# Kernel optimization log

Measured on AMD Instinct MI355X. Metric: run time of the kernel, lower is better.

Reference implementation:

```python
import jax, jax.numpy as jnp
import numpy as np

N = 100_000   # nodes
E = 3_200_000 # edges
B = 64        # graphs in batch
OUT = 64      # config


def setup_inputs() -> dict:
    key = jax.random.key(0)
    ks = jax.random.split(key, 12)
    x = jax.random.normal(ks[0], (N, 3), dtype=jnp.float32)
    edge_index = jax.random.randint(ks[1], (2, E), 0, N, dtype=jnp.int32)
    batch = jnp.sort(jax.random.randint(ks[2], (N,), 0, B, dtype=jnp.int32))
    # GCNConv weights (PyG: out = norm_adj @ (x @ W) + b)
    W1 = jax.random.normal(ks[3], (3, 32), dtype=jnp.float32) * 0.5
    b1 = jnp.zeros((32,), dtype=jnp.float32)
    W2 = jax.random.normal(ks[4], (32, 32), dtype=jnp.float32) * 0.18
    b2 = jnp.zeros((32,), dtype=jnp.float32)
    LW1 = jax.random.normal(ks[5], (64, 64), dtype=jnp.float32) * 0.125
    Lb1 = jnp.zeros((64,), dtype=jnp.float32)
    LW2 = jax.random.normal(ks[6], (64, OUT), dtype=jnp.float32) * 0.125
    Lb2 = jnp.zeros((OUT,), dtype=jnp.float32)
    return {"x": x, "edge_index": edge_index, "batch": batch,
            "W1": W1, "b1": b1, "W2": W2, "b2": b2,
            "LW1": LW1, "Lb1": Lb1, "LW2": LW2, "Lb2": Lb2}


def _gcn_norm(edge_index, n):
    # add self-loops, compute symmetric normalization D^-1/2 (A+I) D^-1/2
    loops = jnp.arange(n, dtype=edge_index.dtype)
    src = jnp.concatenate([edge_index[0], loops])
    dst = jnp.concatenate([edge_index[1], loops])
    deg = jax.ops.segment_sum(jnp.ones_like(dst, dtype=jnp.float32), dst,
                              num_segments=n)
    dinv = jnp.where(deg > 0, 1.0 / jnp.sqrt(deg), 0.0)
    norm = dinv[src] * dinv[dst]  # [E+N]
    return src, dst, norm


def _gcn_conv(x, W, b, src, dst, norm, n):
    h = x @ W                         # [N, F_out] tiny GEMM
    m = h[src] * norm[:, None]        # edge gather  [E+N, F_out]
    out = jax.ops.segment_sum(m, dst, num_segments=n)  # scatter-add
    return out + b


def _pool(x, batch, nb):
    # cat(global_max_pool, global_mean_pool)
    mx = jax.ops.segment_max(x, batch, num_segments=nb)
    sm = jax.ops.segment_sum(x, batch, num_segments=nb)
    cnt = jax.ops.segment_sum(jnp.ones((x.shape[0],), x.dtype), batch,
                              num_segments=nb)
    mean = sm / jnp.maximum(cnt, 1.0)[:, None]
    return jnp.concatenate([mx, mean], axis=1)


def reference(x, edge_index, batch, W1, b1, W2, b2, LW1, Lb1, LW2, Lb2):
    n = x.shape[0]
    src, dst, norm = _gcn_norm(edge_index, n)
    h = jax.nn.relu(_gcn_conv(x, W1, b1, src, dst, norm, n))
    x1 = _pool(h, batch, B)           # [B, 64]
    h2 = jax.nn.relu(_gcn_conv(h, W2, b2, src, dst, norm, n))
    x2 = _pool(h2, batch, B)          # [B, 64]
    z = jax.nn.relu((x1 + x2) @ LW1 + Lb1)
    # dropout p=0.5 skipped (eval mode / training=False)
    out = z @ LW2 + Lb2               # [B, OUT]; .squeeze(1) is a no-op for OUT>1
    return out
```

## Files before the change

### kernel.cpp

```cpp
#include <hip/hip_runtime.h>
#include <hip/hip_fp16.h>


#define F 32
#define POOLD 64
#define BKT 512
#define BKTL2 9
#define EPB 8192
#define MAXBUCK 256

typedef __attribute__((ext_vector_type(8))) _Float16 half8;

__global__ void k_histB(const int* __restrict__ ei, int* __restrict__ bcnt,
                        int e, int nbuck, int nblk) {
    __shared__ int h[MAXBUCK];
    for (int b = threadIdx.x; b < nbuck; b += 256) h[b] = 0;
    __syncthreads();
    int base = blockIdx.x * EPB;
#pragma unroll
    for (int k = 0; k < EPB / 1024; ++k) {
        int i = base + (k * 256 + threadIdx.x) * 4;
        if (i + 4 <= e) {
            int4 d4 = *reinterpret_cast<const int4*>(ei + e + i);
            atomicAdd(&h[d4.x >> BKTL2], 1);
            atomicAdd(&h[d4.y >> BKTL2], 1);
            atomicAdd(&h[d4.z >> BKTL2], 1);
            atomicAdd(&h[d4.w >> BKTL2], 1);
        } else {
            for (int j = i; j < e && j < i + 4; ++j)
                atomicAdd(&h[ei[e + j] >> BKTL2], 1);
        }
    }
    __syncthreads();
    for (int b = threadIdx.x; b < nbuck; b += 256)
        bcnt[b * nblk + blockIdx.x] = h[b];
}

__global__ void k_rowscan(int* __restrict__ bcnt, int* __restrict__ tot, int nblk) {
    __shared__ int lds[256];
    int* row = bcnt + (size_t)blockIdx.x * nblk;
    int t = threadIdx.x;
    int running = 0;
    for (int chunk = 0; chunk < nblk; chunk += 256) {
        int idx = chunk + t;
        int v = (idx < nblk) ? row[idx] : 0;
        lds[t] = v;
        __syncthreads();
        int val = v;
        for (int off = 1; off < 256; off <<= 1) {
            int other = (t >= off) ? lds[t - off] : 0;
            __syncthreads();
            val += other;
            lds[t] = val;
            __syncthreads();
        }
        if (idx < nblk) row[idx] = running + val - v;
        running += lds[255];
        __syncthreads();
    }
    if (t == 0) tot[blockIdx.x] = running;
}

__global__ void k_bscan(const int* __restrict__ tot, int* __restrict__ bstart,
                        int nbuck, int e) {
    __shared__ int lds[256];
    int t = threadIdx.x;
    int v = (t < nbuck) ? tot[t] : 0;
    lds[t] = v;
    __syncthreads();
    int val = v;
    for (int off = 1; off < 256; off <<= 1) {
        int other = (t >= off) ? lds[t - off] : 0;
        __syncthreads();
        val += other;
        lds[t] = val;
        __syncthreads();
    }
    if (t < nbuck) bstart[t] = val - v;
    if (t == 0) bstart[nbuck] = e;
}

__global__ void k_bin(const int* __restrict__ ei, const int* __restrict__ bstart,
                      const int* __restrict__ bcnt, int* __restrict__ packed,
                      int e, int nbuck, int nblk) {
    __shared__ int cur[MAXBUCK];
    for (int b = threadIdx.x; b < nbuck; b += 256)
        cur[b] = bstart[b] + bcnt[b * nblk + blockIdx.x];
    __syncthreads();
    int base = blockIdx.x * EPB;
#pragma unroll
    for (int k = 0; k < EPB / 1024; ++k) {
        int i = base + (k * 256 + threadIdx.x) * 4;
        if (i + 4 <= e) {
            int4 s4 = *reinterpret_cast<const int4*>(ei + i);
            int4 d4 = *reinterpret_cast<const int4*>(ei + e + i);
            int p0 = atomicAdd(&cur[d4.x >> BKTL2], 1);
            int p1 = atomicAdd(&cur[d4.y >> BKTL2], 1);
            int p2 = atomicAdd(&cur[d4.z >> BKTL2], 1);
            int p3 = atomicAdd(&cur[d4.w >> BKTL2], 1);
            packed[p0] = (s4.x << BKTL2) | (d4.x & (BKT - 1));
            packed[p1] = (s4.y << BKTL2) | (d4.y & (BKT - 1));
            packed[p2] = (s4.z << BKTL2) | (d4.z & (BKT - 1));
            packed[p3] = (s4.w << BKTL2) | (d4.w & (BKT - 1));
        } else {
            for (int j = i; j < e && j < i + 4; ++j) {
                int s = ei[j], d = ei[e + j];
                int p = atomicAdd(&cur[d >> BKTL2], 1);
                packed[p] = (s << BKTL2) | (d & (BKT - 1));
            }
        }
    }
}

__global__ void k_place2(const int* __restrict__ packed, const int* __restrict__ bstart,
                         int* __restrict__ col, int* __restrict__ rp,
                         float* __restrict__ dinv, int n) {
    __shared__ int deg[BKT];
    __shared__ int sc[BKT];
    __shared__ int cur[BKT];
    int t = threadIdx.x;
    deg[t] = 0;
    __syncthreads();
    int start = bstart[blockIdx.x];
    int end = bstart[blockIdx.x + 1];
    for (int i = start + t; i < end; i += BKT)
        atomicAdd(&deg[packed[i] & (BKT - 1)], 1);
    __syncthreads();
    int d0 = deg[t];
    sc[t] = d0;
    __syncthreads();
    int val = d0;
    for (int off = 1; off < BKT; off <<= 1) {
        int other = (t >= off) ? sc[t - off] : 0;
        __syncthreads();
        val += other;
        sc[t] = val;
        __syncthreads();
    }
    int node = blockIdx.x * BKT + t;
    int ex = start + val - d0;
    if (node < n) {
        rp[node] = ex;
        dinv[node] = rsqrtf((float)d0 + 1.0f);
    }
    cur[t] = ex;
    __syncthreads();
    for (int i = start + t; i < end; i += BKT) {
        int u = packed[i];
        int p = atomicAdd(&cur[u & (BKT - 1)], 1);
        col[p] = u >> BKTL2;
    }
}

__global__ void k_xw1(const float* __restrict__ x, const float* __restrict__ W1,
                      _Float16* __restrict__ p0, _Float16* __restrict__ p1, int n) {
    int i = blockIdx.x * blockDim.x + threadIdx.x;
    if (i >= n * F) return;
    int node = i >> 5, f = i & (F - 1);
    float x0 = x[node * 3 + 0], x1 = x[node * 3 + 1], x2 = x[node * 3 + 2];
    float v = x0 * W1[f] + x1 * W1[F + f] + x2 * W1[2 * F + f];
    _Float16* plane = (f < 16) ? p0 : p1;
    plane[node * 16 + (f & 15)] = (_Float16)v;
}

__global__ void k_gemm2(const _Float16* __restrict__ h0, const _Float16* __restrict__ h1,
                        const float* __restrict__ W2,
                        _Float16* __restrict__ g0, _Float16* __restrict__ g1, int n) {
    int i = blockIdx.x * blockDim.x + threadIdx.x;
    if (i >= n * F) return;
    int node = i >> 5, f = i & (F - 1);
    const _Float16* r0 = h0 + (size_t)node * 16;
    const _Float16* r1 = h1 + (size_t)node * 16;
    float acc = 0.0f;
#pragma unroll
    for (int k = 0; k < 16; ++k) acc += (float)r0[k] * W2[k * F + f];
#pragma unroll
    for (int k = 0; k < 16; ++k) acc += (float)r1[k] * W2[(k + 16) * F + f];
    _Float16* plane = (f < 16) ? g0 : g1;
    plane[node * 16 + (f & 15)] = (_Float16)acc;
}

__global__ void k_gather(const _Float16* __restrict__ plane, const int* __restrict__ rp,
                         const int* __restrict__ col, const float* __restrict__ dinv,
                         const float* __restrict__ bias, const int* __restrict__ batch,
                         _Float16* __restrict__ outPlane,
                         float* __restrict__ psum, float* __restrict__ pmax,
                         float* __restrict__ cnt, int n, int ne, int fh,
                         int store, int do_cnt) {
    int t = blockIdx.x * blockDim.x + threadIdx.x;
    int node = t >> 1, q = t & 1;
    if (node >= n) return;
    int start = rp[node];
    int end = (node + 1 < n) ? rp[node + 1] : ne;
    float dv = dinv[node];

    half8 hv = *reinterpret_cast<const half8*>(plane + (size_t)node * 16 + q * 8);
    float dvv = dv * dv;
    float acc[8];
#pragma unroll
    for (int j = 0; j < 8; ++j) acc[j] = (float)hv[j] * dvv;

    int e = start;
    for (; e + 8 <= end; e += 8) {
        int s[8];
#pragma unroll
        for (int u = 0; u < 8; ++u) s[u] = col[e + u];
        half8 v[8];
#pragma unroll
        for (int u = 0; u < 8; ++u)
            v[u] = *reinterpret_cast<const half8*>(plane + (size_t)s[u] * 16 + q * 8);
        float w[8];
#pragma unroll
        for (int u = 0; u < 8; ++u) w[u] = dinv[s[u]] * dv;
#pragma unroll
        for (int u = 0; u < 8; ++u)
#pragma unroll
            for (int j = 0; j < 8; ++j) acc[j] += (float)v[u][j] * w[u];
    }
    for (; e < end; ++e) {
        int s = col[e];
        float wv = dinv[s] * dv;
        half8 v = *reinterpret_cast<const half8*>(plane + (size_t)s * 16 + q * 8);
#pragma unroll
        for (int j = 0; j < 8; ++j) acc[j] += (float)v[j] * wv;
    }

    float vv[8];
#pragma unroll
    for (int j = 0; j < 8; ++j)
        vv[j] = fmaxf(acc[j] + bias[fh * 16 + q * 8 + j], 0.0f);
    if (store) {
        half8 o;
#pragma unroll
        for (int j = 0; j < 8; ++j) o[j] = (_Float16)vv[j];
        *reinterpret_cast<half8*>(outPlane + (size_t)node * 16 + q * 8) = o;
    }

    int b = batch[node];
    int lane = threadIdx.x & 63;
    int bFirst = __shfl(b, 0);
    int bLast  = __shfl(b, 63);
    if (bFirst == bLast) {
        float sv[8], mv[8];
#pragma unroll
        for (int j = 0; j < 8; ++j) { sv[j] = vv[j]; mv[j] = vv[j]; }
        for (int off = 2; off < 64; off <<= 1) {
#pragma unroll
            for (int j = 0; j < 8; ++j) {
                sv[j] += __shfl_down(sv[j], off);
                mv[j] = fmaxf(mv[j], __shfl_down(mv[j], off));
            }
        }
        if (lane < 2) {
            float* ps = psum + b * F + fh * 16 + lane * 8;
            int* pm = reinterpret_cast<int*>(pmax + b * F + fh * 16 + lane * 8);
#pragma unroll
            for (int j = 0; j < 8; ++j) {
                atomicAdd(ps + j, sv[j]);
                atomicMax(pm + j, __float_as_int(mv[j]));
            }
            if (do_cnt && lane == 0) atomicAdd(&cnt[b], 32.0f);
        }
    } else {
        float* ps = psum + b * F + fh * 16 + q * 8;
        int* pm = reinterpret_cast<int*>(pmax + b * F + fh * 16 + q * 8);
#pragma unroll
        for (int j = 0; j < 8; ++j) {
            atomicAdd(ps + j, vv[j]);
            atomicMax(pm + j, __float_as_int(vv[j]));
        }
        if (do_cnt && q == 0) atomicAdd(&cnt[b], 1.0f);
    }
}

__global__ void k_mlp(const float* __restrict__ sum1, const float* __restrict__ max1,
                      const float* __restrict__ sum2, const float* __restrict__ max2,
                      const float* __restrict__ cnt,
                      const float* __restrict__ LW1, const float* __restrict__ Lb1,
                      const float* __restrict__ LW2, const float* __restrict__ Lb2,
                      float* __restrict__ out, int outd) {
    __shared__ float zs[POOLD];
    int b = blockIdx.x, j = threadIdx.x;
    float invc = 1.0f / fmaxf(cnt[b], 1.0f);
    float acc = Lb1[j];
#pragma unroll
    for (int i = 0; i < POOLD; ++i) {
        float s;
        if (i < F) s = max1[b * F + i] + max2[b * F + i];
        else       s = (sum1[b * F + i - F] + sum2[b * F + i - F]) * invc;
        acc += s * LW1[i * POOLD + j];
    }
    zs[j] = fmaxf(acc, 0.0f);
    __syncthreads();
    if (j < outd) {
        float a2 = Lb2[j];
#pragma unroll
        for (int jj = 0; jj < POOLD; ++jj) a2 += zs[jj] * LW2[jj * outd + j];
        out[b * outd + j] = a2;
    }
}

extern "C" void kernel_launch(void* const* d_in, const int* in_sizes, int n_in,
                              void* d_out, int out_size, void* d_ws, size_t ws_size,
                              hipStream_t stream) {
    const float* x    = (const float*)d_in[0];
    const int*   ei   = (const int*)d_in[1];
    const int*   batch= (const int*)d_in[2];
    const float* W1   = (const float*)d_in[3];
    const float* b1   = (const float*)d_in[4];
    const float* W2   = (const float*)d_in[5];
    const float* b2   = (const float*)d_in[6];
    const float* LW1  = (const float*)d_in[7];
    const float* Lb1  = (const float*)d_in[8];
    const float* LW2  = (const float*)d_in[9];
    const float* Lb2  = (const float*)d_in[10];
    float* out = (float*)d_out;

    const int N = in_sizes[0] / 3;
    const int E = in_sizes[1] / 2;
    const int OUTD = in_sizes[10];
    const int B = out_size / OUTD;
    const int poolsz = 4 * B * F + B;
    const int NBUCK = (N + BKT - 1) / BKT;
    const int NBLK = (E + EPB - 1) / EPB;

    char* p = (char*)d_ws;
    float* pools= (float*)p;          p += (size_t)poolsz * 4;
    int* bcnt   = (int*)p;            p += (size_t)NBUCK * NBLK * 4;
    int* tot    = (int*)p;            p += (size_t)MAXBUCK * 4;
    int* bstart = (int*)p;            p += (size_t)(NBUCK + 1) * 4;
    int* rowptr = (int*)p;            p += (size_t)N * 4;
    int* col    = (int*)p;            p += (size_t)E * 4;
    float* dinv = (float*)p;          p += (size_t)N * 4;
    _Float16* b0p0 = (_Float16*)p;    p += (size_t)N * 16 * 2;
    _Float16* b0p1 = (_Float16*)p;    p += (size_t)N * 16 * 2;
    _Float16* b1p0 = (_Float16*)p;    p += (size_t)N * 16 * 2;
    _Float16* b1p1 = (_Float16*)p;    p += (size_t)N * 16 * 2;
    int* packed = (int*)b0p0;
    float* sum1 = pools;
    float* max1 = sum1 + B * F;
    float* sum2 = max1 + B * F;
    float* max2 = sum2 + B * F;
    float* cnt  = max2 + B * F;

    const int BS = 256;
    auto g1 = [&](long long n) { return (int)((n + BS - 1) / BS); };

    hipMemsetAsync(pools, 0, (size_t)poolsz * 4, stream);
    k_histB<<<NBLK, BS, 0, stream>>>(ei, bcnt, E, NBUCK, NBLK);
    k_rowscan<<<NBUCK, 256, 0, stream>>>(bcnt, tot, NBLK);
    k_bscan<<<1, 256, 0, stream>>>(tot, bstart, NBUCK, E);
    k_bin<<<NBLK, BS, 0, stream>>>(ei, bstart, bcnt, packed, E, NBUCK, NBLK);
    k_place2<<<NBUCK, BKT, 0, stream>>>(packed, bstart, col, rowptr, dinv, N);

    k_xw1<<<g1((long long)N * F), BS, 0, stream>>>(x, W1, b0p0, b0p1, N);
    k_gather<<<g1((long long)N * 2), BS, 0, stream>>>(b0p0, rowptr, col, dinv, b1,
                                                      batch, b1p0, sum1, max1, cnt,
                                                      N, E, 0, 1, 1);
    k_gather<<<g1((long long)N * 2), BS, 0, stream>>>(b0p1, rowptr, col, dinv, b1,
                                                      batch, b1p1, sum1, max1, cnt,
                                                      N, E, 1, 1, 0);
    k_gemm2<<<g1((long long)N * F), BS, 0, stream>>>(b1p0, b1p1, W2, b0p0, b0p1, N);
    k_gather<<<g1((long long)N * 2), BS, 0, stream>>>(b0p0, rowptr, col, dinv, b2,
                                                      batch, b1p0, sum2, max2, cnt,
                                                      N, E, 0, 0, 0);
    k_gather<<<g1((long long)N * 2), BS, 0, stream>>>(b0p1, rowptr, col, dinv, b2,
                                                      batch, b1p1, sum2, max2, cnt,
                                                      N, E, 1, 0, 0);

    k_mlp<<<B, 64, 0, stream>>>(sum1, max1, sum2, max2, cnt,
                                LW1, Lb1, LW2, Lb2, out, OUTD);
}
```

Baseline: 389.8 us.

## Merge per-plane gather launches and split each node's edges across two lanes

```diff
diff --git a/kernel.cpp b/kernel.cpp
--- a/kernel.cpp
+++ b/kernel.cpp
@@ -180,96 +180,108 @@
     plane[node * 16 + (f & 15)] = (_Float16)acc;
 }
 
-__global__ void k_gather(const _Float16* __restrict__ plane, const int* __restrict__ rp,
-                         const int* __restrict__ col, const float* __restrict__ dinv,
-                         const float* __restrict__ bias, const int* __restrict__ batch,
-                         _Float16* __restrict__ outPlane,
-                         float* __restrict__ psum, float* __restrict__ pmax,
-                         float* __restrict__ cnt, int n, int ne, int fh,
-                         int store, int do_cnt) {
-    int t = blockIdx.x * blockDim.x + threadIdx.x;
-    int node = t >> 1, q = t & 1;
+__global__ void k_gather2(const _Float16* __restrict__ pl0, const _Float16* __restrict__ pl1,
+                          const int* __restrict__ rp, const int* __restrict__ col,
+                          const float* __restrict__ dinv, const float* __restrict__ bias,
+                          const int* __restrict__ batch,
+                          _Float16* __restrict__ out0, _Float16* __restrict__ out1,
+                          float* __restrict__ psum, float* __restrict__ pmax,
+                          float* __restrict__ cnt, int n, int ne, int nPB,
+                          int store, int do_cnt) {
+    int grp = blockIdx.x >> 3, sub = blockIdx.x & 7;
+    int plane = sub >> 2;
+    int lb = grp * 4 + (sub & 3);
+    if (lb >= nPB) return;
+    int t = threadIdx.x;
+    int node = (lb << 6) + (t >> 2);
+    int q = (t >> 1) & 1, r = t & 1;
     if (node >= n) return;
+
+    const _Float16* hin = plane ? pl1 : pl0;
     int start = rp[node];
     int end = (node + 1 < n) ? rp[node + 1] : ne;
     float dv = dinv[node];
 
-    half8 hv = *reinterpret_cast<const half8*>(plane + (size_t)node * 16 + q * 8);
-    float dvv = dv * dv;
     float acc[8];
-#pragma unroll
-    for (int j = 0; j < 8; ++j) acc[j] = (float)hv[j] * dvv;
-
-    int e = start;
-    for (; e + 8 <= end; e += 8) {
-        int s[8];
-#pragma unroll
-        for (int u = 0; u < 8; ++u) s[u] = col[e + u];
-        half8 v[8];
-#pragma unroll
-        for (int u = 0; u < 8; ++u)
-            v[u] = *reinterpret_cast<const half8*>(plane + (size_t)s[u] * 16 + q * 8);
-        float w[8];
-#pragma unroll
-        for (int u = 0; u < 8; ++u) w[u] = dinv[s[u]] * dv;
-#pragma unroll
-        for (int u = 0; u < 8; ++u)
-#pragma unroll
-            for (int j = 0; j < 8; ++j) acc[j] += (float)v[u][j] * w[u];
-    }
-    for (; e < end; ++e) {
+    {
+        half8 hv = *reinterpret_cast<const half8*>(hin + (size_t)node * 16 + q * 8);
+        float dvv = (r == 0) ? dv * dv : 0.0f;
+#pragma unroll
+        for (int j = 0; j < 8; ++j) acc[j] = (float)hv[j] * dvv;
+    }
+
+    int e = start + r;
+    for (; e + 6 < end; e += 8) {
+        int s0 = col[e], s1 = col[e + 2], s2 = col[e + 4], s3 = col[e + 6];
+        half8 v0 = *reinterpret_cast<const half8*>(hin + (size_t)s0 * 16 + q * 8);
+        half8 v1 = *reinterpret_cast<const half8*>(hin + (size_t)s1 * 16 + q * 8);
+        half8 v2 = *reinterpret_cast<const half8*>(hin + (size_t)s2 * 16 + q * 8);
+        half8 v3 = *reinterpret_cast<const half8*>(hin + (size_t)s3 * 16 + q * 8);
+        float w0 = dinv[s0] * dv, w1 = dinv[s1] * dv,
+              w2 = dinv[s2] * dv, w3 = dinv[s3] * dv;
+#pragma unroll
+        for (int j = 0; j < 8; ++j)
+            acc[j] += (float)v0[j] * w0 + (float)v1[j] * w1 +
+                      (float)v2[j] * w2 + (float)v3[j] * w3;
+    }
+    for (; e < end; e += 2) {
         int s = col[e];
         float wv = dinv[s] * dv;
-        half8 v = *reinterpret_cast<const half8*>(plane + (size_t)s * 16 + q * 8);
+        half8 v = *reinterpret_cast<const half8*>(hin + (size_t)s * 16 + q * 8);
 #pragma unroll
         for (int j = 0; j < 8; ++j) acc[j] += (float)v[j] * wv;
     }
 
+#pragma unroll
+    for (int j = 0; j < 8; ++j) acc[j] += __shfl_xor(acc[j], 1);
+
     float vv[8];
 #pragma unroll
     for (int j = 0; j < 8; ++j)
-        vv[j] = fmaxf(acc[j] + bias[fh * 16 + q * 8 + j], 0.0f);
-    if (store) {
+        vv[j] = fmaxf(acc[j] + bias[plane * 16 + q * 8 + j], 0.0f);
+
+    if (store && r == 0) {
+        _Float16* hout = plane ? out1 : out0;
         half8 o;
 #pragma unroll
         for (int j = 0; j < 8; ++j) o[j] = (_Float16)vv[j];
-        *reinterpret_cast<half8*>(outPlane + (size_t)node * 16 + q * 8) = o;
+        *reinterpret_cast<half8*>(hout + (size_t)node * 16 + q * 8) = o;
     }
 
     int b = batch[node];
-    int lane = threadIdx.x & 63;
+    int lane = t & 63;
     int bFirst = __shfl(b, 0);
     int bLast  = __shfl(b, 63);
     if (bFirst == bLast) {
         float sv[8], mv[8];
 #pragma unroll
         for (int j = 0; j < 8; ++j) { sv[j] = vv[j]; mv[j] = vv[j]; }
-        for (int off = 2; off < 64; off <<= 1) {
+        for (int off = 4; off < 64; off <<= 1) {
 #pragma unroll
             for (int j = 0; j < 8; ++j) {
                 sv[j] += __shfl_down(sv[j], off);
                 mv[j] = fmaxf(mv[j], __shfl_down(mv[j], off));
             }
         }
-        if (lane < 2) {
-            float* ps = psum + b * F + fh * 16 + lane * 8;
-            int* pm = reinterpret_cast<int*>(pmax + b * F + fh * 16 + lane * 8);
+        if (lane < 4 && r == 0) {
+            float* ps = psum + b * F + plane * 16 + q * 8;
+            int* pm = reinterpret_cast<int*>(pmax + b * F + plane * 16 + q * 8);
 #pragma unroll
             for (int j = 0; j < 8; ++j) {
                 atomicAdd(ps + j, sv[j]);
                 atomicMax(pm + j, __float_as_int(mv[j]));
             }
-            if (do_cnt && lane == 0) atomicAdd(&cnt[b], 32.0f);
-        }
-    } else {
-        float* ps = psum + b * F + fh * 16 + q * 8;
-        int* pm = reinterpret_cast<int*>(pmax + b * F + fh * 16 + q * 8);
+            if (do_cnt && plane == 0 && lane == 0) atomicAdd(&cnt[b], 16.0f);
+        }
+    } else if (r == 0) {
+        float* ps = psum + b * F + plane * 16 + q * 8;
+        int* pm = reinterpret_cast<int*>(pmax + b * F + plane * 16 + q * 8);
 #pragma unroll
         for (int j = 0; j < 8; ++j) {
             atomicAdd(ps + j, vv[j]);
             atomicMax(pm + j, __float_as_int(vv[j]));
         }
-        if (do_cnt && q == 0) atomicAdd(&cnt[b], 1.0f);
+        if (do_cnt && plane == 0 && q == 0) atomicAdd(&cnt[b], 1.0f);
     }
 }
 
@@ -323,6 +335,7 @@
     const int poolsz = 4 * B * F + B;
     const int NBUCK = (N + BKT - 1) / BKT;
     const int NBLK = (E + EPB - 1) / EPB;
+    const int NPB = (N + 63) / 64;
 
     char* p = (char*)d_ws;
     float* pools= (float*)p;          p += (size_t)poolsz * 4;
@@ -345,6 +358,7 @@
 
     const int BS = 256;
     auto g1 = [&](long long n) { return (int)((n + BS - 1) / BS); };
+    const int gatherBlocks = ((NPB + 3) / 4) * 8;
 
     hipMemsetAsync(pools, 0, (size_t)poolsz * 4, stream);
     k_histB<<<NBLK, BS, 0, stream>>>(ei, bcnt, E, NBUCK, NBLK);
@@ -354,19 +368,13 @@
     k_place2<<<NBUCK, BKT, 0, stream>>>(packed, bstart, col, rowptr, dinv, N);
 
     k_xw1<<<g1((long long)N * F), BS, 0, stream>>>(x, W1, b0p0, b0p1, N);
-    k_gather<<<g1((long long)N * 2), BS, 0, stream>>>(b0p0, rowptr, col, dinv, b1,
-                                                      batch, b1p0, sum1, max1, cnt,
-                                                      N, E, 0, 1, 1);
-    k_gather<<<g1((long long)N * 2), BS, 0, stream>>>(b0p1, rowptr, col, dinv, b1,
-                                                      batch, b1p1, sum1, max1, cnt,
-                                                      N, E, 1, 1, 0);
+    k_gather2<<<gatherBlocks, BS, 0, stream>>>(b0p0, b0p1, rowptr, col, dinv, b1,
+                                               batch, b1p0, b1p1, sum1, max1, cnt,
+                                               N, E, NPB, 1, 1);
     k_gemm2<<<g1((long long)N * F), BS, 0, stream>>>(b1p0, b1p1, W2, b0p0, b0p1, N);
-    k_gather<<<g1((long long)N * 2), BS, 0, stream>>>(b0p0, rowptr, col, dinv, b2,
-                                                      batch, b1p0, sum2, max2, cnt,
-                                                      N, E, 0, 0, 0);
-    k_gather<<<g1((long long)N * 2), BS, 0, stream>>>(b0p1, rowptr, col, dinv, b2,
-                                                      batch, b1p1, sum2, max2, cnt,
-                                                      N, E, 1, 0, 0);
+    k_gather2<<<gatherBlocks, BS, 0, stream>>>(b0p0, b0p1, rowptr, col, dinv, b2,
+                                               batch, b1p0, b1p1, sum2, max2, cnt,
+                                               N, E, NPB, 0, 0);
 
     k_mlp<<<B, 64, 0, stream>>>(sum1, max1, sum2, max2, cnt,
                                 LW1, Lb1, LW2, Lb2, out, OUTD);
```

Result: faster. 369.1 us (-5.3%).
